# Kernel tuning notes

Hardware: AMD Instinct MI355X
Metric: run time of the kernel (lower is better)

The kernel has to match this reference:

```python
import jax, jax.numpy as jnp
import numpy as np

SEQ, DM, NH, DH = 8192, 1024, 16, 64


def setup_inputs() -> dict:
    key = jax.random.key(0)
    k = jax.random.split(key, 8)
    return {
        "xs": jax.random.normal(k[0], (SEQ, DM), dtype=jnp.float32),
        "wq": jax.random.normal(k[1], (NH, DH, DM), dtype=jnp.float32),
        "wk": jax.random.normal(k[2], (NH, DH, DM), dtype=jnp.float32),
        "wv": jax.random.normal(k[3], (NH, DH, DM), dtype=jnp.float32),
        # MLP: Linear(NH*DH -> DM), gelu, Linear(DM -> NH*DH); eqx stores W as (out, in)
        "w1": jax.random.normal(k[4], (DM, NH * DH), dtype=jnp.float32) * 0.02,
        "b1": jnp.zeros((DM,), dtype=jnp.float32),
        "w2": jax.random.normal(k[5], (NH * DH, DM), dtype=jnp.float32) * 0.02,
        "b2": jnp.zeros((NH * DH,), dtype=jnp.float32),
    }


def _act(x):
    return jax.nn.elu(x) + 1.0


def reference(xs, wq, wk, wv, w1, b1, w2, b2):
    # project: (n_heads d_head d_model),(seq d_model) -> (seq n_heads d_head)
    q = jnp.einsum('hdm,sm->shd', wq, xs)
    k = jnp.einsum('hdm,sm->shd', wk, xs)
    v = jnp.einsum('hdm,sm->shd', wv, xs)

    def cell(state, qkv):
        s, z = state                      # s: (h, dk, dv), z: (h, dk)
        qt, kt, vt = qkv                  # each (h, d)
        kt = _act(kt)
        s = s + jnp.einsum('hk,hv->hkv', kt, vt)
        z = z + kt
        qa = _act(qt)
        # faithful to einops 'n_heads d_head_k d_head_v, n_heads d_head_q -> n_heads d_head_v'
        sq = jnp.einsum('hkv,hq->hv', s, qa)
        zq = jnp.einsum('hk,hq->h', z, qa)
        return (s, z), sq / zq[:, None]

    init = (jnp.zeros((NH, DH, DH), xs.dtype), jnp.zeros((NH, DH), xs.dtype))
    _, out = jax.lax.scan(cell, init, (q, k, v))   # out: (seq, h, d)
    out = out.reshape(SEQ, NH * DH)
    h = jax.nn.gelu(out @ w1.T + b1)
    return h @ w2.T + b2
```

## Files before the change

### kernel.cpp

```cpp
#include <hip/hip_runtime.h>
#include <hip/hip_bf16.h>

using bf16 = __hip_bfloat16;
typedef __attribute__((ext_vector_type(8))) short shortx8;
typedef __attribute__((ext_vector_type(4))) float f32x4;

#define SEQ 8192
#define DM 1024
#define NH 16
#define CHUNK 64
#define NC (SEQ / CHUNK)

__device__ __forceinline__ void load_lds16(const bf16* g, bf16* l) {
    __builtin_amdgcn_global_load_lds(
        (const __attribute__((address_space(1))) void*)g,
        (__attribute__((address_space(3))) void*)l, 16, 0, 0);
}

__device__ __forceinline__ float bf2f(short s) {
    union { unsigned u; float f; } x;
    x.u = ((unsigned)(unsigned short)s) << 16;
    return x.f;
}

__global__ __launch_bounds__(256) void convert_all(const float* __restrict__ xs,
                                                   const float* __restrict__ wk,
                                                   const float* __restrict__ wv,
                                                   const float* __restrict__ w1,
                                                   const float* __restrict__ w2,
                                                   bf16* __restrict__ xsb,
                                                   bf16* __restrict__ wall) {
    const int b = blockIdx.x;
    const float* in;
    bf16* out;
    int blk;
    if (b < 8192) {
        in = xs; out = xsb; blk = b;
    } else {
        const int seg = (b - 8192) >> 10;
        blk = (b - 8192) & 1023;
        out = wall + (size_t)seg * DM * DM;
        if (seg == 0)      in = wk;
        else if (seg == 1) in = wv;
        else if (seg == 2) in = w1;
        else               in = w2;
    }
    size_t i = ((size_t)blk * 256 + threadIdx.x) * 4;
    float4 f = *(const float4*)(in + i);
    out[i + 0] = __float2bfloat16(f.x);
    out[i + 1] = __float2bfloat16(f.y);
    out[i + 2] = __float2bfloat16(f.z);
    out[i + 3] = __float2bfloat16(f.w);
}

template <int MODE>
__global__ __launch_bounds__(256) void gemm_nt(const bf16* __restrict__ A,
                                               const bf16* __restrict__ B,
                                               void* __restrict__ Cv,
                                               const float* __restrict__ bias,
                                               float* __restrict__ kappa,
                                               float* __restrict__ numbuf,
                                               float* __restrict__ denbuf,
                                               int M, int N, int K) {
    __shared__ bf16 As[128][64];
    __shared__ bf16 Bs[128][64];
    __shared__ float Ksh[4][64];

    const int tid  = threadIdx.x;
    const int L    = blockIdx.x + blockIdx.y * gridDim.x;
    const int ry   = L % gridDim.y;
    const int rx   = L / gridDim.y;
    const int bm   = ry * 128;
    const int bn   = rx * 128;
    const int wave = tid >> 6;
    const int lane = tid & 63;
    const int wm   = (wave >> 1) * 64;
    const int wn   = (wave & 1) * 64;
    const int quad = lane >> 4;
    const int m16  = lane & 15;
    const int r7   = m16 & 7;

    f32x4 acc[4][4];
    #pragma unroll
    for (int i = 0; i < 4; ++i)
        #pragma unroll
        for (int j = 0; j < 4; ++j)
            #pragma unroll
            for (int r = 0; r < 4; ++r) acc[i][j][r] = 0.f;

    for (int k0 = 0; k0 < K; k0 += 64) {
        #pragma unroll
        for (int it = 0; it < 4; ++it) {
            int s = it * 256 + tid;
            int row = s >> 3, pos = s & 7;
            int g = pos ^ (row & 7);
            load_lds16(A + (size_t)(bm + row) * K + k0 + g * 8, &As[row][pos * 8]);
            load_lds16(B + (size_t)(bn + row) * K + k0 + g * 8, &Bs[row][pos * 8]);
        }
        __syncthreads();

        #pragma unroll
        for (int kx = 0; kx < 2; ++kx) {
            const int p = ((kx << 2) + quad) ^ r7;
            shortx8 af[4], bfr[4];
            #pragma unroll
            for (int i = 0; i < 4; ++i)
                af[i] = *(const shortx8*)&As[wm + i * 16 + m16][p * 8];
            #pragma unroll
            for (int j = 0; j < 4; ++j)
                bfr[j] = *(const shortx8*)&Bs[wn + j * 16 + m16][p * 8];
            #pragma unroll
            for (int i = 0; i < 4; ++i)
                #pragma unroll
                for (int j = 0; j < 4; ++j)
                    acc[i][j] = __builtin_amdgcn_mfma_f32_16x16x32_bf16(af[i], bfr[j], acc[i][j], 0, 0, 0);
        }
        __syncthreads();
    }

    if (MODE == 0) {
        const int h = (bn + wn) >> 6;
        #pragma unroll
        for (int i = 0; i < 4; ++i) {
            #pragma unroll
            for (int r = 0; r < 4; ++r) {
                float s = 0.f;
                #pragma unroll
                for (int j = 0; j < 4; ++j) {
                    float v = acc[i][j][r];
                    s += v > 0.f ? v + 1.f : __expf(v);
                }
                s += __shfl_xor(s, 1);
                s += __shfl_xor(s, 2);
                s += __shfl_xor(s, 4);
                s += __shfl_xor(s, 8);
                if (m16 == 0)
                    kappa[(size_t)h * SEQ + bm + wm + i * 16 + quad * 4 + r] = s;
            }
        }
        return;
    }

    if (MODE == 1) {
        const int c = (bm + wm) >> 6;
        const int h = (bn + wn) >> 6;
        float kv = kappa[(size_t)h * SEQ + bm + wm + lane];
        Ksh[wave][lane] = kv;
        float dsum = kv;
        #pragma unroll
        for (int off = 32; off > 0; off >>= 1) dsum += __shfl_xor(dsum, off);
        if (lane == 0) denbuf[(size_t)h * NC + c] = dsum;

        float s[4] = {0.f, 0.f, 0.f, 0.f};
        #pragma unroll
        for (int i = 0; i < 4; ++i) {
            #pragma unroll
            for (int r = 0; r < 4; ++r) {
                float kr = Ksh[wave][i * 16 + quad * 4 + r];
                #pragma unroll
                for (int j = 0; j < 4; ++j) s[j] += kr * acc[i][j][r];
            }
        }
        #pragma unroll
        for (int j = 0; j < 4; ++j) {
            s[j] += __shfl_xor(s[j], 16);
            s[j] += __shfl_xor(s[j], 32);
        }
        if (quad == 0) {
            size_t nb = ((size_t)h * NC + c) * 64;
            #pragma unroll
            for (int j = 0; j < 4; ++j) numbuf[nb + j * 16 + m16] = s[j];
        }
    }

    #pragma unroll
    for (int i = 0; i < 4; ++i) {
        int row0 = bm + wm + i * 16 + quad * 4;
        #pragma unroll
        for (int j = 0; j < 4; ++j) {
            int col = bn + wn + j * 16 + m16;
            #pragma unroll
            for (int r = 0; r < 4; ++r) {
                float v = acc[i][j][r];
                size_t o = (size_t)(row0 + r) * N + col;
                if (MODE == 1) {
                    ((bf16*)Cv)[o] = __float2bfloat16(v);
                } else if (MODE == 2) {
                    v += bias[col];
                    float t = tanhf(0.7978845608028654f * (v + 0.044715f * v * v * v));
                    ((bf16*)Cv)[o] = __float2bfloat16(0.5f * v * (1.f + t));
                } else {
                    v += bias[col];
                    ((float*)Cv)[o] = v;
                }
            }
        }
    }
}

__global__ __launch_bounds__(256) void prefix_state(float* __restrict__ numbuf,
                                                    float* __restrict__ denbuf) {
    const int h = blockIdx.x;
    const int wave = threadIdx.x >> 6;
    const int d = threadIdx.x & 63;
    __shared__ float tot[4][64];
    __shared__ float dtot[4];

    float val[32], dval[32];
    const int c0 = wave * 32;
    #pragma unroll
    for (int i = 0; i < 32; ++i) {
        size_t idx = (size_t)h * NC + c0 + i;
        val[i]  = numbuf[idx * 64 + d];
        dval[i] = denbuf[idx];
    }
    float run = 0.f, drun = 0.f;
    #pragma unroll
    for (int i = 0; i < 32; ++i) {
        float t = val[i];  val[i]  = run;  run  += t;
        float dt = dval[i]; dval[i] = drun; drun += dt;
    }
    tot[wave][d] = run;
    if (d == 0) dtot[wave] = drun;
    __syncthreads();
    float off = 0.f, doff = 0.f;
    for (int w = 0; w < wave; ++w) { off += tot[w][d]; doff += dtot[w]; }
    #pragma unroll
    for (int i = 0; i < 32; ++i) {
        size_t idx = (size_t)h * NC + c0 + i;
        numbuf[idx * 64 + d] = val[i] + off;
        if (d == 0) denbuf[idx] = dval[i] + doff;
    }
}

__global__ __launch_bounds__(256) void chunk_out(const bf16* __restrict__ vb,
                                                 const float* __restrict__ kappa,
                                                 const float* __restrict__ numbuf,
                                                 const float* __restrict__ denbuf,
                                                 bf16* __restrict__ out) {
    const int h = blockIdx.x, c = blockIdx.y;
    __shared__ float Ksh[64];
    __shared__ float Vs[64][64];
    const int tid = threadIdx.x;

    #pragma unroll
    for (int it = 0; it < 2; ++it) {
        int s = it * 256 + tid;
        int r = s >> 3, d8 = (s & 7) * 8;
        shortx8 raw = *(const shortx8*)(vb + (size_t)(c * 64 + r) * DM + h * 64 + d8);
        #pragma unroll
        for (int e = 0; e < 8; ++e) Vs[r][d8 + e] = bf2f(raw[e]);
    }
    if (tid < 64) Ksh[tid] = kappa[(size_t)h * SEQ + c * 64 + tid];
    __syncthreads();

    const int t  = tid >> 2;
    const int v0 = (tid & 3) << 4;
    const size_t bidx = (size_t)h * NC + c;

    float den = denbuf[bidx];
    float num[16];
    #pragma unroll
    for (int jj = 0; jj < 4; ++jj) {
        float4 n4 = *(const float4*)&numbuf[bidx * 64 + v0 + jj * 4];
        num[jj * 4 + 0] = n4.x; num[jj * 4 + 1] = n4.y;
        num[jj * 4 + 2] = n4.z; num[jj * 4 + 3] = n4.w;
    }

    for (int i = 0; i <= t; ++i) {
        float s = Ksh[i];
        den += s;
        #pragma unroll
        for (int jj = 0; jj < 4; ++jj) {
            float4 v4 = *(const float4*)&Vs[i][v0 + jj * 4];
            num[jj * 4 + 0] += s * v4.x; num[jj * 4 + 1] += s * v4.y;
            num[jj * 4 + 2] += s * v4.z; num[jj * 4 + 3] += s * v4.w;
        }
    }

    const float inv = 1.0f / den;
    size_t og = (size_t)(c * 64 + t) * DM + h * 64 + v0;
    #pragma unroll
    for (int j = 0; j < 16; ++j) out[og + j] = __float2bfloat16(num[j] * inv);
}

extern "C" void kernel_launch(void* const* d_in, const int* in_sizes, int n_in,
                              void* d_out, int out_size, void* d_ws, size_t ws_size,
                              hipStream_t stream) {
    const float* xs = (const float*)d_in[0];
    const float* wk = (const float*)d_in[2];
    const float* wv = (const float*)d_in[3];
    const float* w1 = (const float*)d_in[4];
    const float* b1 = (const float*)d_in[5];
    const float* w2 = (const float*)d_in[6];
    const float* b2 = (const float*)d_in[7];
    float* y = (float*)d_out;

    char* base = (char*)d_ws;
    size_t off = 0;
    auto alloc = [&](size_t b) -> char* {
        char* p = base + off;
        off += (b + 255) & ~(size_t)255;
        return p;
    };

    const size_t NMAT = (size_t)SEQ * DM;
    const size_t NW   = (size_t)DM * DM;
    bf16*  xsb    = (bf16*)alloc(NMAT * 2);
    bf16*  wall   = (bf16*)alloc(4 * NW * 2);
    bf16*  wkb    = wall;
    bf16*  wvb    = wall + NW;
    bf16*  w1b    = wall + 2 * NW;
    bf16*  w2b    = wall + 3 * NW;
    bf16*  vb     = (bf16*)alloc(NMAT * 2);
    float* kappa  = (float*)alloc((size_t)NH * SEQ * 4);
    float* numbuf = (float*)alloc((size_t)NH * NC * 64 * 4);
    float* denbuf = (float*)alloc((size_t)NH * NC * 4);
    bf16*  outb   = (bf16*)alloc(NMAT * 2);
    bf16*  hb     = (bf16*)alloc(NMAT * 2);

    convert_all<<<8192 + 4 * 1024, 256, 0, stream>>>(xs, wk, wv, w1, w2,
                                                     xsb, wall);

    dim3 ggrid(DM / 128, SEQ / 128);
    gemm_nt<0><<<ggrid, 256, 0, stream>>>(xsb, wkb, nullptr, nullptr, kappa,
                                          nullptr, nullptr, SEQ, DM, DM);
    gemm_nt<1><<<ggrid, 256, 0, stream>>>(xsb, wvb, vb, nullptr, kappa,
                                          numbuf, denbuf, SEQ, DM, DM);

    prefix_state<<<NH, 256, 0, stream>>>(numbuf, denbuf);
    chunk_out<<<dim3(NH, NC), 256, 0, stream>>>(vb, kappa, numbuf, denbuf, outb);

    gemm_nt<2><<<ggrid, 256, 0, stream>>>(outb, w1b, hb, b1, nullptr,
                                          nullptr, nullptr, SEQ, DM, DM);
    gemm_nt<3><<<ggrid, 256, 0, stream>>>(hb, w2b, y, b2, nullptr,
                                          nullptr, nullptr, SEQ, DM, DM);
}
```

Measured before the change: 230.0 us.

## Replace 128x128 GEMM with pipelined 256x256 tile kernel and fuse K/V projections

Replaces the 128x128 single-buffered GEMM with a 512-thread 256x256 tile kernel. The new kernel double-buffers LDS, interleaves the next tile's global-to-LDS loads with MFMA quarters, raises wave priority during MFMA and swizzles workgroup order across XCDs. The K and V projections now run as one N=2048 GEMM over the concatenated weights. The per-chunk numerator and denominator reduction moves out of the V epilogue into a separate chunk_sums kernel. This aims at better data reuse and load/compute overlap, at the cost of an extra launch and a re-read of V, and the larger tiles give only 128 workgroups for the 1024-wide GEMMs.

```diff
diff --git a/kernel.cpp b/kernel.cpp
--- a/kernel.cpp
+++ b/kernel.cpp
@@ -10,6 +10,7 @@
 #define NH 16
 #define CHUNK 64
 #define NC (SEQ / CHUNK)
+#define NT (DM / 64)
 
 __device__ __forceinline__ void load_lds16(const bf16* g, bf16* l) {
     __builtin_amdgcn_global_load_lds(
@@ -21,6 +22,12 @@
     union { unsigned u; float f; } x;
     x.u = ((unsigned)(unsigned short)s) << 16;
     return x.f;
+}
+
+__device__ __forceinline__ void barrier_raw() {
+    asm volatile("" ::: "memory");
+    __builtin_amdgcn_s_barrier();
+    asm volatile("" ::: "memory");
 }
 
 __global__ __launch_bounds__(256) void convert_all(const float* __restrict__ xs,
@@ -54,147 +61,239 @@
 }
 
 template <int MODE>
-__global__ __launch_bounds__(256) void gemm_nt(const bf16* __restrict__ A,
-                                               const bf16* __restrict__ B,
-                                               void* __restrict__ Cv,
-                                               const float* __restrict__ bias,
-                                               float* __restrict__ kappa,
-                                               float* __restrict__ numbuf,
-                                               float* __restrict__ denbuf,
-                                               int M, int N, int K) {
-    __shared__ bf16 As[128][64];
-    __shared__ bf16 Bs[128][64];
-    __shared__ float Ksh[4][64];
-
-    const int tid  = threadIdx.x;
-    const int L    = blockIdx.x + blockIdx.y * gridDim.x;
-    const int ry   = L % gridDim.y;
-    const int rx   = L / gridDim.y;
-    const int bm   = ry * 128;
-    const int bn   = rx * 128;
+__global__ __launch_bounds__(512, 2) void gemm256(const bf16* __restrict__ A,
+                                                  const bf16* __restrict__ B,
+                                                  void* __restrict__ Cv,
+                                                  const float* __restrict__ bias,
+                                                  float* __restrict__ kappa,
+                                                  int N) {
+    __shared__ bf16 As[2][256][64];
+    __shared__ bf16 Bs[2][256][64];
+
+    const int tid = threadIdx.x;
+    const int nwg = gridDim.x * gridDim.y;
+    const int bid = blockIdx.x + blockIdx.y * gridDim.x;
+    const int cpx = nwg >> 3;
+    const int swz = (bid & 7) * cpx + (bid >> 3);
+    const int ry  = swz % gridDim.y;
+    const int rx  = swz / gridDim.y;
+    const int bm  = ry * 256;
+    const int bn  = rx * 256;
+
     const int wave = tid >> 6;
     const int lane = tid & 63;
-    const int wm   = (wave >> 1) * 64;
-    const int wn   = (wave & 1) * 64;
+    const int wr   = wave >> 2;
+    const int wc   = wave & 3;
     const int quad = lane >> 4;
     const int m16  = lane & 15;
     const int r7   = m16 & 7;
-
-    f32x4 acc[4][4];
-    #pragma unroll
-    for (int i = 0; i < 4; ++i)
-        #pragma unroll
-        for (int j = 0; j < 4; ++j)
-            #pragma unroll
-            for (int r = 0; r < 4; ++r) acc[i][j][r] = 0.f;
-
-    for (int k0 = 0; k0 < K; k0 += 64) {
-        #pragma unroll
-        for (int it = 0; it < 4; ++it) {
-            int s = it * 256 + tid;
+    const int wr128 = wr * 128;
+    const int wc64  = wc * 64;
+    const int kp0 = (quad ^ r7) * 8;
+    const int kp1 = ((4 + quad) ^ r7) * 8;
+
+    auto stageA = [&](int half, int kt) {
+        #pragma unroll
+        for (int it = 0; it < 2; ++it) {
+            int s = it * 512 + tid;
             int row = s >> 3, pos = s & 7;
             int g = pos ^ (row & 7);
-            load_lds16(A + (size_t)(bm + row) * K + k0 + g * 8, &As[row][pos * 8]);
-            load_lds16(B + (size_t)(bn + row) * K + k0 + g * 8, &Bs[row][pos * 8]);
-        }
-        __syncthreads();
-
-        #pragma unroll
-        for (int kx = 0; kx < 2; ++kx) {
-            const int p = ((kx << 2) + quad) ^ r7;
-            shortx8 af[4], bfr[4];
-            #pragma unroll
-            for (int i = 0; i < 4; ++i)
-                af[i] = *(const shortx8*)&As[wm + i * 16 + m16][p * 8];
-            #pragma unroll
-            for (int j = 0; j < 4; ++j)
-                bfr[j] = *(const shortx8*)&Bs[wn + j * 16 + m16][p * 8];
-            #pragma unroll
-            for (int i = 0; i < 4; ++i)
+            load_lds16(A + (size_t)(bm + half * 128 + row) * DM + kt * 64 + g * 8,
+                       &As[kt & 1][half * 128 + row][pos * 8]);
+        }
+    };
+    auto stageB = [&](int half, int kt) {
+        #pragma unroll
+        for (int it = 0; it < 2; ++it) {
+            int s = it * 512 + tid;
+            int row = s >> 3, pos = s & 7;
+            int g = pos ^ (row & 7);
+            load_lds16(B + (size_t)(bn + half * 128 + row) * DM + kt * 64 + g * 8,
+                       &Bs[kt & 1][half * 128 + row][pos * 8]);
+        }
+    };
+
+    f32x4 acc[8][4];
+    #pragma unroll
+    for (int i = 0; i < 8; ++i)
+        #pragma unroll
+        for (int j = 0; j < 4; ++j)
+            #pragma unroll
+            for (int r = 0; r < 4; ++r) acc[i][j][r] = 0.f;
+
+    stageA(0, 0); stageA(1, 0); stageB(0, 0); stageB(1, 0);
+    stageB(0, 1); stageB(1, 1);
+    asm volatile("s_waitcnt vmcnt(4)" ::: "memory");
+    barrier_raw();
+
+    shortx8 af[4][2], blo[2][2], bhi[2][2];
+
+    #pragma unroll 1
+    for (int t = 0; t < NT; ++t) {
+        const int sl = t & 1;
+        #pragma unroll
+        for (int i = 0; i < 4; ++i) {
+            af[i][0] = *(const shortx8*)&As[sl][wr128 + i * 16 + m16][kp0];
+            af[i][1] = *(const shortx8*)&As[sl][wr128 + i * 16 + m16][kp1];
+        }
+        #pragma unroll
+        for (int j = 0; j < 2; ++j) {
+            blo[j][0] = *(const shortx8*)&Bs[sl][wc64 + j * 16 + m16][kp0];
+            blo[j][1] = *(const shortx8*)&Bs[sl][wc64 + j * 16 + m16][kp1];
+        }
+        if (t + 1 < NT) stageA(0, t + 1);
+        barrier_raw();
+        __builtin_amdgcn_s_setprio(1);
+        #pragma unroll
+        for (int i = 0; i < 4; ++i)
+            #pragma unroll
+            for (int j = 0; j < 2; ++j) {
+                acc[i][j] = __builtin_amdgcn_mfma_f32_16x16x32_bf16(af[i][0], blo[j][0], acc[i][j], 0, 0, 0);
+                acc[i][j] = __builtin_amdgcn_mfma_f32_16x16x32_bf16(af[i][1], blo[j][1], acc[i][j], 0, 0, 0);
+            }
+        __builtin_amdgcn_s_setprio(0);
+        barrier_raw();
+
+        #pragma unroll
+        for (int j = 0; j < 2; ++j) {
+            bhi[j][0] = *(const shortx8*)&Bs[sl][wc64 + (j + 2) * 16 + m16][kp0];
+            bhi[j][1] = *(const shortx8*)&Bs[sl][wc64 + (j + 2) * 16 + m16][kp1];
+        }
+        if (t + 1 < NT) stageA(1, t + 1);
+        barrier_raw();
+        __builtin_amdgcn_s_setprio(1);
+        #pragma unroll
+        for (int i = 0; i < 4; ++i)
+            #pragma unroll
+            for (int j = 0; j < 2; ++j) {
+                acc[i][j + 2] = __builtin_amdgcn_mfma_f32_16x16x32_bf16(af[i][0], bhi[j][0], acc[i][j + 2], 0, 0, 0);
+                acc[i][j + 2] = __builtin_amdgcn_mfma_f32_16x16x32_bf16(af[i][1], bhi[j][1], acc[i][j + 2], 0, 0, 0);
+            }
+        __builtin_amdgcn_s_setprio(0);
+        barrier_raw();
+
+        #pragma unroll
+        for (int i = 0; i < 4; ++i) {
+            af[i][0] = *(const shortx8*)&As[sl][wr128 + 64 + i * 16 + m16][kp0];
+            af[i][1] = *(const shortx8*)&As[sl][wr128 + 64 + i * 16 + m16][kp1];
+        }
+        if (t + 2 < NT) stageB(0, t + 2);
+        barrier_raw();
+        __builtin_amdgcn_s_setprio(1);
+        #pragma unroll
+        for (int i = 0; i < 4; ++i)
+            #pragma unroll
+            for (int j = 0; j < 2; ++j) {
+                acc[4 + i][j] = __builtin_amdgcn_mfma_f32_16x16x32_bf16(af[i][0], blo[j][0], acc[4 + i][j], 0, 0, 0);
+                acc[4 + i][j] = __builtin_amdgcn_mfma_f32_16x16x32_bf16(af[i][1], blo[j][1], acc[4 + i][j], 0, 0, 0);
+            }
+        __builtin_amdgcn_s_setprio(0);
+        barrier_raw();
+
+        if (t + 2 < NT) {
+            stageB(1, t + 2);
+            asm volatile("s_waitcnt vmcnt(4)" ::: "memory");
+        } else {
+            asm volatile("s_waitcnt vmcnt(0)" ::: "memory");
+        }
+        barrier_raw();
+        __builtin_amdgcn_s_setprio(1);
+        #pragma unroll
+        for (int i = 0; i < 4; ++i)
+            #pragma unroll
+            for (int j = 0; j < 2; ++j) {
+                acc[4 + i][j + 2] = __builtin_amdgcn_mfma_f32_16x16x32_bf16(af[i][0], bhi[j][0], acc[4 + i][j + 2], 0, 0, 0);
+                acc[4 + i][j + 2] = __builtin_amdgcn_mfma_f32_16x16x32_bf16(af[i][1], bhi[j][1], acc[4 + i][j + 2], 0, 0, 0);
+            }
+        __builtin_amdgcn_s_setprio(0);
+        barrier_raw();
+    }
+
+    if (MODE == 0) {
+        const int gcol0 = bn + wc64;
+        if (gcol0 < DM) {
+            const int h = gcol0 >> 6;
+            #pragma unroll
+            for (int i = 0; i < 8; ++i) {
                 #pragma unroll
-                for (int j = 0; j < 4; ++j)
-                    acc[i][j] = __builtin_amdgcn_mfma_f32_16x16x32_bf16(af[i], bfr[j], acc[i][j], 0, 0, 0);
-        }
-        __syncthreads();
-    }
-
-    if (MODE == 0) {
-        const int h = (bn + wn) >> 6;
-        #pragma unroll
-        for (int i = 0; i < 4; ++i) {
-            #pragma unroll
-            for (int r = 0; r < 4; ++r) {
-                float s = 0.f;
+                for (int r = 0; r < 4; ++r) {
+                    float s = 0.f;
+                    #pragma unroll
+                    for (int j = 0; j < 4; ++j) {
+                        float v = acc[i][j][r];
+                        s += v > 0.f ? v + 1.f : __expf(v);
+                    }
+                    s += __shfl_xor(s, 1);
+                    s += __shfl_xor(s, 2);
+                    s += __shfl_xor(s, 4);
+                    s += __shfl_xor(s, 8);
+                    if (m16 == 0)
+                        kappa[(size_t)h * SEQ + bm + wr128 + i * 16 + quad * 4 + r] = s;
+                }
+            }
+        } else {
+            bf16* vb = (bf16*)Cv;
+            #pragma unroll
+            for (int i = 0; i < 8; ++i) {
+                int row0 = bm + wr128 + i * 16 + quad * 4;
                 #pragma unroll
                 for (int j = 0; j < 4; ++j) {
-                    float v = acc[i][j][r];
-                    s += v > 0.f ? v + 1.f : __expf(v);
+                    int col = gcol0 - DM + j * 16 + m16;
+                    #pragma unroll
+                    for (int r = 0; r < 4; ++r)
+                        vb[(size_t)(row0 + r) * DM + col] = __float2bfloat16(acc[i][j][r]);
                 }
-                s += __shfl_xor(s, 1);
-                s += __shfl_xor(s, 2);
-                s += __shfl_xor(s, 4);
-                s += __shfl_xor(s, 8);
-                if (m16 == 0)
-                    kappa[(size_t)h * SEQ + bm + wm + i * 16 + quad * 4 + r] = s;
             }
         }
         return;
     }
 
-    if (MODE == 1) {
-        const int c = (bm + wm) >> 6;
-        const int h = (bn + wn) >> 6;
-        float kv = kappa[(size_t)h * SEQ + bm + wm + lane];
-        Ksh[wave][lane] = kv;
-        float dsum = kv;
-        #pragma unroll
-        for (int off = 32; off > 0; off >>= 1) dsum += __shfl_xor(dsum, off);
-        if (lane == 0) denbuf[(size_t)h * NC + c] = dsum;
-
-        float s[4] = {0.f, 0.f, 0.f, 0.f};
-        #pragma unroll
-        for (int i = 0; i < 4; ++i) {
+    #pragma unroll
+    for (int i = 0; i < 8; ++i) {
+        int row0 = bm + wr128 + i * 16 + quad * 4;
+        #pragma unroll
+        for (int j = 0; j < 4; ++j) {
+            int col = bn + wc64 + j * 16 + m16;
+            float bv = bias[col];
             #pragma unroll
             for (int r = 0; r < 4; ++r) {
-                float kr = Ksh[wave][i * 16 + quad * 4 + r];
-                #pragma unroll
-                for (int j = 0; j < 4; ++j) s[j] += kr * acc[i][j][r];
-            }
-        }
-        #pragma unroll
-        for (int j = 0; j < 4; ++j) {
-            s[j] += __shfl_xor(s[j], 16);
-            s[j] += __shfl_xor(s[j], 32);
-        }
-        if (quad == 0) {
-            size_t nb = ((size_t)h * NC + c) * 64;
-            #pragma unroll
-            for (int j = 0; j < 4; ++j) numbuf[nb + j * 16 + m16] = s[j];
-        }
-    }
-
-    #pragma unroll
-    for (int i = 0; i < 4; ++i) {
-        int row0 = bm + wm + i * 16 + quad * 4;
-        #pragma unroll
-        for (int j = 0; j < 4; ++j) {
-            int col = bn + wn + j * 16 + m16;
-            #pragma unroll
-            for (int r = 0; r < 4; ++r) {
-                float v = acc[i][j][r];
-                size_t o = (size_t)(row0 + r) * N + col;
-                if (MODE == 1) {
-                    ((bf16*)Cv)[o] = __float2bfloat16(v);
-                } else if (MODE == 2) {
-                    v += bias[col];
-                    float t = tanhf(0.7978845608028654f * (v + 0.044715f * v * v * v));
-                    ((bf16*)Cv)[o] = __float2bfloat16(0.5f * v * (1.f + t));
+                float v = acc[i][j][r] + bv;
+                if (MODE == 2) {
+                    float tt = tanhf(0.7978845608028654f * (v + 0.044715f * v * v * v));
+                    ((bf16*)Cv)[(size_t)(row0 + r) * N + col] = __float2bfloat16(0.5f * v * (1.f + tt));
                 } else {
-                    v += bias[col];
-                    ((float*)Cv)[o] = v;
+                    ((float*)Cv)[(size_t)(row0 + r) * N + col] = v;
                 }
             }
         }
+    }
+}
+
+__global__ __launch_bounds__(256) void chunk_sums(const bf16* __restrict__ vb,
+                                                  const float* __restrict__ kappa,
+                                                  float* __restrict__ numbuf,
+                                                  float* __restrict__ denbuf) {
+    const int h = blockIdx.x, c = blockIdx.y;
+    const int v = threadIdx.x & 63, tq = threadIdx.x >> 6;
+    __shared__ float red[4][64];
+    __shared__ float dred[4];
+    float np = 0.f, dp = 0.f;
+    #pragma unroll
+    for (int i = 0; i < 16; ++i) {
+        int t = c * 64 + tq * 16 + i;
+        float kv = kappa[(size_t)h * SEQ + t];
+        float vv = bf2f(((const short*)vb)[(size_t)t * DM + h * 64 + v]);
+        np += kv * vv;
+        dp += kv;
+    }
+    red[tq][v] = np;
+    if (v == 0) dred[tq] = dp;
+    __syncthreads();
+    if (tq == 0) {
+        float s = red[0][v] + red[1][v] + red[2][v] + red[3][v];
+        numbuf[((size_t)h * NC + c) * 64 + v] = s;
+        if (v == 0)
+            denbuf[(size_t)h * NC + c] = dred[0] + dred[1] + dred[2] + dred[3];
     }
 }
 
@@ -308,8 +407,6 @@
     const size_t NW   = (size_t)DM * DM;
     bf16*  xsb    = (bf16*)alloc(NMAT * 2);
     bf16*  wall   = (bf16*)alloc(4 * NW * 2);
-    bf16*  wkb    = wall;
-    bf16*  wvb    = wall + NW;
     bf16*  w1b    = wall + 2 * NW;
     bf16*  w2b    = wall + 3 * NW;
     bf16*  vb     = (bf16*)alloc(NMAT * 2);
@@ -322,17 +419,15 @@
     convert_all<<<8192 + 4 * 1024, 256, 0, stream>>>(xs, wk, wv, w1, w2,
                                                      xsb, wall);
 
-    dim3 ggrid(DM / 128, SEQ / 128);
-    gemm_nt<0><<<ggrid, 256, 0, stream>>>(xsb, wkb, nullptr, nullptr, kappa,
-                                          nullptr, nullptr, SEQ, DM, DM);
-    gemm_nt<1><<<ggrid, 256, 0, stream>>>(xsb, wvb, vb, nullptr, kappa,
-                                          numbuf, denbuf, SEQ, DM, DM);
-
+    gemm256<0><<<dim3(2048 / 256, SEQ / 256), 512, 0, stream>>>(
+        xsb, wall, vb, nullptr, kappa, 2048);
+
+    chunk_sums<<<dim3(NH, NC), 256, 0, stream>>>(vb, kappa, numbuf, denbuf);
     prefix_state<<<NH, 256, 0, stream>>>(numbuf, denbuf);
     chunk_out<<<dim3(NH, NC), 256, 0, stream>>>(vb, kappa, numbuf, denbuf, outb);
 
-    gemm_nt<2><<<ggrid, 256, 0, stream>>>(outb, w1b, hb, b1, nullptr,
-                                          nullptr, nullptr, SEQ, DM, DM);
-    gemm_nt<3><<<ggrid, 256, 0, stream>>>(hb, w2b, y, b2, nullptr,
-                                          nullptr, nullptr, SEQ, DM, DM);
-}
+    gemm256<2><<<dim3(DM / 256, SEQ / 256), 512, 0, stream>>>(
+        outb, w1b, hb, b1, nullptr, DM);
+    gemm256<3><<<dim3(DM / 256, SEQ / 256), 512, 0, stream>>>(
+        hb, w2b, y, b2, nullptr, DM);
+}
```

After: 285.4 us. +24.1%, slower.
